# Performance work log

Hardware: AMD Instinct MI355X
Metric: run time of the kernel (lower is better)

Reference implementation:

```python
import jax, jax.numpy as jnp
import numpy as np

B, M, K, KNN = 2, 256, 64, 16
CXYZ, CFEAT = 3, 61
CIN = CXYZ + CFEAT  # 64
MLPS = [64, 128]
SUMM = sum(MLPS)    # 192
CALIB = 64
EXP = [256, 512]
OUT = 256
EPS = 1e-5


def bn(x, g, b):
    # BatchNorm eval mode with running_mean=0, running_var=1 (channel axis 1)
    shape = (1, -1) + (1,) * (x.ndim - 2)
    return x * (g / jnp.sqrt(1.0 + EPS)).reshape(shape) + b.reshape(shape)


def knn(x, k):
    xx = jnp.sum(x * x, axis=1)                      # (B, N)
    inner = jnp.einsum('bcn,bcm->bnm', x, x)         # (B, N, N)
    pd = 2.0 * inner - xx[:, :, None] - xx[:, None, :]
    return jax.lax.top_k(pd, k)[1]                   # (B, N, k)


def graph_feature(x, idx):
    # x: (B, C, N), idx: (B, N, k) -> (B, 2C, N, k)
    xt = jnp.transpose(x, (0, 2, 1))                 # (B, N, C)
    nb = jax.vmap(lambda a, i: a[i])(xt, idx)        # (B, N, k, C)
    ctr = xt[:, :, None, :]
    feat = jnp.concatenate([nb - ctr, jnp.broadcast_to(ctr, nb.shape)], axis=-1)
    return jnp.transpose(feat, (0, 3, 1, 2))


def forward(xyz, feats, e1_w, e1_g, e1_b, e2_w, e2_g, e2_b,
            cal1_w, cal1_g, cal1_b, cal2_w, cal2_bias,
            exp1_w, exp1_g, exp1_b, exp2_w, exp2_g, exp2_b,
            red_w, red_g, red_b, sc1_w, sc1_b, sc2_w, sc2_b,
            sc_n1_g, sc_n1_b, sc_n2_g, sc_n2_b):
    x3 = xyz.reshape(B * M, K, CXYZ).transpose(0, 2, 1)      # (BM, 3, K)
    f = feats.reshape(B * M, K, CFEAT).transpose(0, 2, 1)    # (BM, 61, K)
    idx = knn(x3, KNN)                                        # USE_FEATS_DIS=False: knn once on xyz
    x = jnp.concatenate([x3, f], axis=1)                      # (BM, 64, K)
    outs = []
    for W, g, b in ((e1_w, e1_g, e1_b), (e2_w, e2_g, e2_b)):
        gf = graph_feature(x, idx)                            # (BM, 2C, K, knn)
        y = jax.nn.relu(bn(jnp.einsum('oc,bcnk->bonk', W, gf), g, b))
        x = y.max(axis=-1)                                    # (BM, mlp_i, K)
        outs.append(x)
    x = jnp.concatenate(outs, axis=1)                         # (BM, 192, K)
    c = jax.nn.relu(bn(jnp.einsum('oc,bcn->bon', cal1_w, x), cal1_g, cal1_b))
    c = jnp.einsum('oc,bcn->bon', cal2_w, c) + cal2_bias[None, :, None]
    x = jax.nn.sigmoid(c) * x
    x = jax.nn.relu(bn(jnp.einsum('oc,bcn->bon', exp1_w, x), exp1_g, exp1_b))
    x = jax.nn.relu(bn(jnp.einsum('oc,bcn->bon', exp2_w, x), exp2_g, exp2_b))
    x = x.max(axis=-1).reshape(B, M, EXP[1]).transpose(0, 2, 1)  # (B, 512, M)
    x = jax.nn.relu(bn(jnp.einsum('oc,bcm->bom', red_w, x), red_g, red_b))
    x = bn(x + x, sc_n1_g, sc_n1_b)
    h = jax.nn.relu(jnp.einsum('oc,bcm->bom', sc1_w, x) + sc1_b[None, :, None])
    h = jnp.einsum('oc,bcm->bom', sc2_w, h) + sc2_b[None, :, None]
    x = bn(x + h, sc_n2_g, sc_n2_b)
    return x                                                  # (B, 256, M)


def setup_inputs() -> dict:
    key = jax.random.key(0)
    ks = jax.random.split(key, 16)
    w = lambda k, s: jax.random.normal(k, s, jnp.float32) * 0.05
    ones = lambda n: jnp.ones((n,), jnp.float32)
    zeros = lambda n: jnp.zeros((n,), jnp.float32)
    return {
        'xyz': jax.random.normal(ks[0], (B, M, K, CXYZ), jnp.float32),
        'feats': jax.random.normal(ks[1], (B, M, K, CFEAT), jnp.float32),
        'e1_w': w(ks[2], (MLPS[0], 2 * CIN)), 'e1_g': ones(MLPS[0]), 'e1_b': zeros(MLPS[0]),
        'e2_w': w(ks[3], (MLPS[1], 2 * MLPS[0])), 'e2_g': ones(MLPS[1]), 'e2_b': zeros(MLPS[1]),
        'cal1_w': w(ks[4], (CALIB, SUMM)), 'cal1_g': ones(CALIB), 'cal1_b': zeros(CALIB),
        'cal2_w': w(ks[5], (SUMM, CALIB)), 'cal2_bias': zeros(SUMM),
        'exp1_w': w(ks[6], (EXP[0], SUMM)), 'exp1_g': ones(EXP[0]), 'exp1_b': zeros(EXP[0]),
        'exp2_w': w(ks[7], (EXP[1], EXP[0])), 'exp2_g': ones(EXP[1]), 'exp2_b': zeros(EXP[1]),
        'red_w': w(ks[8], (OUT, EXP[1])), 'red_g': ones(OUT), 'red_b': zeros(OUT),
        'sc1_w': w(ks[9], (OUT, OUT)), 'sc1_b': zeros(OUT),
        'sc2_w': w(ks[10], (OUT, OUT)), 'sc2_b': zeros(OUT),
        'sc_n1_g': ones(OUT), 'sc_n1_b': zeros(OUT),
        'sc_n2_g': ones(OUT), 'sc_n2_b': zeros(OUT),
    }


def reference(xyz, feats, e1_w, e1_g, e1_b, e2_w, e2_g, e2_b,
              cal1_w, cal1_g, cal1_b, cal2_w, cal2_bias,
              exp1_w, exp1_g, exp1_b, exp2_w, exp2_g, exp2_b,
              red_w, red_g, red_b, sc1_w, sc1_b, sc2_w, sc2_b,
              sc_n1_g, sc_n1_b, sc_n2_g, sc_n2_b):
    return forward(xyz, feats, e1_w, e1_g, e1_b, e2_w, e2_g, e2_b,
                   cal1_w, cal1_g, cal1_b, cal2_w, cal2_bias,
                   exp1_w, exp1_g, exp1_b, exp2_w, exp2_g, exp2_b,
                   red_w, red_g, red_b, sc1_w, sc1_b, sc2_w, sc2_b,
                   sc_n1_g, sc_n1_b, sc_n2_g, sc_n2_b)
```

## Files before the change

### kernel.cpp

```cpp
#include <hip/hip_runtime.h>
#include <hip/hip_bf16.h>
#include <math.h>
#include <stddef.h>

#define DEV __device__ __forceinline__
__device__ const float BNS = 0.99999500003749968f;

typedef __bf16 bf16x8 __attribute__((ext_vector_type(8)));
typedef float  f32x4  __attribute__((ext_vector_type(4)));

#define MF(a,b,c) __builtin_amdgcn_mfma_f32_16x16x32_bf16(a,b,c,0,0,0)

DEV unsigned short f2bs(float v){
  union{ __hip_bfloat16 b; unsigned short u; } c; c.b=__float2bfloat16(v); return c.u;
}
DEV float bs2f(unsigned short u){
  union{ unsigned short u; __hip_bfloat16 b; } c; c.u=u; return __bfloat162float(c.b);
}

DEV void put_split4(unsigned short* chunks, int n, int c0, const float* v){
  int cc=c0>>5, u=(c0>>3)&3, e=c0&7;
  unsigned short* base = chunks + cc*4096;
  unsigned short h0=f2bs(v[0]), h1=f2bs(v[1]), h2=f2bs(v[2]), h3=f2bs(v[3]);
  ushort4 hq = make_ushort4(h0,h1,h2,h3);
  ushort4 lq = make_ushort4(f2bs(v[0]-bs2f(h0)), f2bs(v[1]-bs2f(h1)),
                            f2bs(v[2]-bs2f(h2)), f2bs(v[3]-bs2f(h3)));
  *(ushort4*)&base[(n*8 + (u     ^ (n&7)))*8 + e] = hq;
  *(ushort4*)&base[(n*8 + ((u+4) ^ (n&7)))*8 + e] = lq;
}
DEV void get_split4(const unsigned short* chunks, int n, int c0, float* v){
  int cc=c0>>5, u=(c0>>3)&3, e=c0&7;
  const unsigned short* base = chunks + cc*4096;
  ushort4 hq = *(const ushort4*)&base[(n*8 + (u     ^ (n&7)))*8 + e];
  ushort4 lq = *(const ushort4*)&base[(n*8 + ((u+4) ^ (n&7)))*8 + e];
  v[0]=bs2f(hq.x)+bs2f(lq.x); v[1]=bs2f(hq.y)+bs2f(lq.y);
  v[2]=bs2f(hq.z)+bs2f(lq.z); v[3]=bs2f(hq.w)+bs2f(lq.w);
}


__global__ __launch_bounds__(256) void k_prep(const float* __restrict__ e1_w,
    const float* __restrict__ e2_w, const float* __restrict__ cal1_w,
    const float* __restrict__ cal2_w, const float* __restrict__ exp1_w,
    const float* __restrict__ exp2_w, unsigned short* __restrict__ Whi,
    unsigned short* __restrict__ Wlo,
    const float* __restrict__ red_w, const float* __restrict__ sc1_w,
    const float* __restrict__ sc2_w, float* __restrict__ Wt_red,
    float* __restrict__ Wt_s1, float* __restrict__ Wt_s2){
  __shared__ float s[32][33];
  int bid = blockIdx.x;
  if(bid < 896){
    const float* src; unsigned short *hi,*lo; int mode, O=0, i0;
    if(bid<32)      { src=e1_w;  hi=Whi;       lo=Wlo;       mode=1; O= 64; i0=bid*256; }
    else if(bid<96) { src=e2_w;  hi=Whi+8192;  lo=Wlo+8192;  mode=1; O=128; i0=(bid-32)*256; }
    else if(bid<144){ src=cal1_w;hi=Whi+24576; lo=Wlo+24576; mode=0;        i0=(bid-96)*256; }
    else if(bid<192){ src=cal2_w;hi=Whi+36864; lo=Wlo+36864; mode=0;        i0=(bid-144)*256; }
    else if(bid<384){ src=exp1_w;hi=Whi+49152; lo=Wlo+49152; mode=0;        i0=(bid-192)*256; }
    else            { src=exp2_w;hi=Whi+98304; lo=Wlo+98304; mode=0;        i0=(bid-384)*256; }
    int i = i0 + threadIdx.x;
    float v;
    if(mode==0) v = src[i];
    else {
      int row=i>>6, c=i&63;
      v = (row<O) ? src[row*128+c] : (src[(row-O)*128+64+c]-src[(row-O)*128+c]);
    }
    unsigned short h=f2bs(v); hi[i]=h; lo[i]=f2bs(v-bs2f(h));
  } else {
    int lb = bid-896;
    const float* in; float* out; int O,K;
    if(lb<128){ in=red_w; out=Wt_red; O=256; K=512; }
    else if(lb<192){ in=sc1_w; out=Wt_s1; O=256; K=256; lb-=128; }
    else { in=sc2_w; out=Wt_s2; O=256; K=256; lb-=192; }
    int nt=O>>5;
    int to=lb%nt, tk=lb/nt;
    int c=threadIdx.x&31, r8=threadIdx.x>>5;
    #pragma unroll
    for(int p=0;p<4;p++){
      int r=r8+p*8;
      s[r][c]=in[(size_t)(to*32+r)*K + tk*32 + c];
    }
    __syncthreads();
    #pragma unroll
    for(int p=0;p<4;p++){
      int r=r8+p*8;
      out[(size_t)(tk*32+r)*O + to*32 + c]=s[c][r];
    }
  }
}

__global__ __launch_bounds__(256) void k_knne12(const float* __restrict__ xyz,
    const float* __restrict__ feats,
    const unsigned short* __restrict__ W1h, const unsigned short* __restrict__ W1l,
    const unsigned short* __restrict__ W2h, const unsigned short* __restrict__ W2l,
    const float* __restrict__ g1, const float* __restrict__ b1,
    const float* __restrict__ g2, const float* __restrict__ b2,
    unsigned short* __restrict__ cat){
  __shared__ float bufA[64*65];
  __shared__ float bufB[64*65];
  __shared__ __align__(16) unsigned short sb[64*136];
  __shared__ int   ips[64*16];
  __shared__ float sx0[64], sx1[64], sx2[64], sxx[64];
  int bm = blockIdx.x;
  int tid = threadIdx.x, n = tid&63, s = tid>>6;
  int wid = tid>>6, lane = tid&63;
  int l15 = lane&15, q = lane>>4;
  if(s==0){
    const float* xp = xyz + (size_t)(bm*64+n)*3;
    float px=xp[0], py=xp[1], pz=xp[2];
    sx0[n]=px; sx1[n]=py; sx2[n]=pz; sxx[n]=px*px+py*py+pz*pz;
  }
  __syncthreads();
  {
    int p = lane>>2, seg = lane&3;
    int n1 = wid*16 + p;
    float px=sx0[n1], py=sx1[n1], pz=sx2[n1], xxn=sxx[n1];
    float pdr[16];
    #pragma unroll
    for(int t=0;t<16;t++){
      int m = seg*16+t;
      pdr[t] = 2.f*(px*sx0[m]+py*sx1[m]+pz*sx2[m]) - xxn - sxx[m];
    }
    for(int j=0;j<16;j++){
      float bv=-3.4e38f; int bi=seg*16;
      #pragma unroll
      for(int t=0;t<16;t++){ if(pdr[t]>bv){bv=pdr[t]; bi=seg*16+t;} }
      float ov=__shfl_xor(bv,1); int oi=__shfl_xor(bi,1);
      if(ov>bv || (ov==bv && oi<bi)){bv=ov;bi=oi;}
      ov=__shfl_xor(bv,2); oi=__shfl_xor(bi,2);
      if(ov>bv || (ov==bv && oi<bi)){bv=ov;bi=oi;}
      if(seg==0) ips[n1*16+j]=bi;
      if((bi>>4)==seg) pdr[bi&15]=-3.4e38f;
    }
  }
  {
    unsigned short* r = sb + n*136;
    if(s==0){
      float px=sx0[n], py=sx1[n], pz=sx2[n];
      unsigned short h;
      h=f2bs(px); r[0]=h; r[64]=f2bs(px-bs2f(h));
      h=f2bs(py); r[1]=h; r[65]=f2bs(py-bs2f(h));
      h=f2bs(pz); r[2]=h; r[66]=f2bs(pz-bs2f(h));
    }
    const float* fp = feats + (size_t)(bm*64+n)*61;
    #pragma unroll
    for(int t=0;t<16;t++){
      int cc = s*16+t;
      if(cc<61){
        float v=fp[cc]; unsigned short h=f2bs(v);
        r[3+cc]=h; r[64+3+cc]=f2bs(v-bs2f(h));
      }
    }
  }
  __syncthreads();
  {
    int rbase = ((wid<2)?0:64) + (wid&1)*32;
    f32x4 acc[2][4];
    #pragma unroll
    for(int a=0;a<2;a++)
      #pragma unroll
      for(int d=0;d<4;d++) acc[a][d]=(f32x4){0.f,0.f,0.f,0.f};
    #pragma unroll
    for(int kc=0;kc<2;kc++){
      int k0=kc*32;
      size_t a0=(size_t)(rbase+l15)*64 + k0 + q*8;
      size_t a1=(size_t)(rbase+16+l15)*64 + k0 + q*8;
      bf16x8 a0h=*(const bf16x8*)(W1h+a0), a0l=*(const bf16x8*)(W1l+a0);
      bf16x8 a1h=*(const bf16x8*)(W1h+a1), a1l=*(const bf16x8*)(W1l+a1);
      #pragma unroll
      for(int nt=0;nt<4;nt++){
        int row = nt*16 + l15;
        bf16x8 bh = *(const bf16x8*)&sb[row*136 + k0 + q*8];
        bf16x8 bl = *(const bf16x8*)&sb[row*136 + 64 + k0 + q*8];
        acc[0][nt]=MF(a0h,bh,acc[0][nt]);
        acc[0][nt]=MF(a0h,bl,acc[0][nt]);
        acc[0][nt]=MF(a0l,bh,acc[0][nt]);
        acc[1][nt]=MF(a1h,bh,acc[1][nt]);
        acc[1][nt]=MF(a1h,bl,acc[1][nt]);
        acc[1][nt]=MF(a1l,bh,acc[1][nt]);
      }
    }
    __syncthreads();
    float* dst = (wid<2)? bufA : bufB;
    int ro = (wid&1)*32;
    #pragma unroll
    for(int mt=0;mt<2;mt++)
      #pragma unroll
      for(int nt=0;nt<4;nt++)
        #pragma unroll
        for(int rr=0;rr<4;rr++)
          dst[(ro+mt*16+q*4+rr)*65 + nt*16+l15] = acc[mt][nt][rr];
  }
  __syncthreads();
  {
    int o = lane;
    float sc = g1[o]*BNS, bi = b1[o];
    #pragma unroll 4
    for(int j=0;j<16;j++){
      int nn = wid*16 + j;
      const int* ip = &ips[nn*16];
      float mz = -3.4e38f;
      #pragma unroll
      for(int k=0;k<16;k++) mz = fmaxf(mz, bufA[o*65 + ip[k]]);
      float v = fmaxf(sc*(mz + bufB[o*65 + nn]) + bi, 0.f);
      unsigned short hv = f2bs(v), lv = f2bs(v - bs2f(hv));
      size_t cb = ((size_t)bm*64+nn)*384 + o;
      cat[cb] = hv; cat[cb+192] = lv;
      sb[nn*136 + o] = hv; sb[nn*136 + 64 + o] = lv;
    }
  }
  for(int ch=0; ch<2; ch++){
    __syncthreads();
    int rbase = ((wid<2)?0:128) + ch*64 + (wid&1)*32;
    f32x4 acc[2][4];
    #pragma unroll
    for(int a=0;a<2;a++)
      #pragma unroll
      for(int d=0;d<4;d++) acc[a][d]=(f32x4){0.f,0.f,0.f,0.f};
    #pragma unroll
    for(int kc=0;kc<2;kc++){
      int k0=kc*32;
      size_t a0=(size_t)(rbase+l15)*64 + k0 + q*8;
      size_t a1=(size_t)(rbase+16+l15)*64 + k0 + q*8;
      bf16x8 a0h=*(const bf16x8*)(W2h+a0), a0l=*(const bf16x8*)(W2l+a0);
      bf16x8 a1h=*(const bf16x8*)(W2h+a1), a1l=*(const bf16x8*)(W2l+a1);
      #pragma unroll
      for(int nt=0;nt<4;nt++){
        int row = nt*16 + l15;
        bf16x8 bh = *(const bf16x8*)&sb[row*136 + k0 + q*8];
        bf16x8 bl = *(const bf16x8*)&sb[row*136 + 64 + k0 + q*8];
        acc[0][nt]=MF(a0h,bh,acc[0][nt]);
        acc[0][nt]=MF(a0h,bl,acc[0][nt]);
        acc[0][nt]=MF(a0l,bh,acc[0][nt]);
        acc[1][nt]=MF(a1h,bh,acc[1][nt]);
        acc[1][nt]=MF(a1h,bl,acc[1][nt]);
        acc[1][nt]=MF(a1l,bh,acc[1][nt]);
      }
    }
    __syncthreads();
    float* dst = (wid<2)? bufA : bufB;
    int ro = (wid&1)*32;
    #pragma unroll
    for(int mt=0;mt<2;mt++)
      #pragma unroll
      for(int nt=0;nt<4;nt++)
        #pragma unroll
        for(int rr=0;rr<4;rr++)
          dst[(ro+mt*16+q*4+rr)*65 + nt*16+l15] = acc[mt][nt][rr];
    __syncthreads();
    int o = ch*64 + lane;
    float sc = g2[o]*BNS, bi = b2[o];
    #pragma unroll 4
    for(int j=0;j<16;j++){
      int nn = wid*16 + j;
      const int* ip = &ips[nn*16];
      float mz = -3.4e38f;
      #pragma unroll
      for(int k=0;k<16;k++) mz = fmaxf(mz, bufA[lane*65 + ip[k]]);
      float v = fmaxf(sc*(mz + bufB[lane*65 + nn]) + bi, 0.f);
      unsigned short hv = f2bs(v);
      size_t cb = ((size_t)bm*64+nn)*384 + 64 + o;
      cat[cb] = hv; cat[cb+192] = f2bs(v - bs2f(hv));
    }
  }
}

__global__ __launch_bounds__(512,4) void k_mlp(
    const unsigned short* __restrict__ Whi, const unsigned short* __restrict__ Wlo,
    const unsigned short* __restrict__ cats,
    const float* __restrict__ c1g, const float* __restrict__ c1b,
    const float* __restrict__ c2bias,
    const float* __restrict__ e1g, const float* __restrict__ e1b,
    const float* __restrict__ e2g, const float* __restrict__ e2b,
    float* __restrict__ pool){
  __shared__ __align__(16) unsigned short buf[8*4096];
  __shared__ __align__(16) unsigned short calB[2*4096];
  int bm = blockIdx.x;
  int tid = threadIdx.x, wid = tid>>6, lane = tid&63;
  int l15 = lane&15, q = lane>>4;

  const unsigned short* w1h = Whi + 24576;
  const unsigned short* w1l = Wlo + 24576;
  int c1ot = wid>>1, c1rh = wid&1;
  size_t c1wo0 = (size_t)(c1ot*16+l15)*192 + q*8;
  bf16x8 cah = *(const bf16x8*)(w1h+c1wo0);
  bf16x8 cal_ = *(const bf16x8*)(w1l+c1wo0);

  size_t xb = (size_t)bm*24576;
  #pragma unroll
  for(int i=0;i<6;i++){
    int U = tid + i*512;
    int kc = U>>9, w = U&511, rr = w>>3, up = w&7, u = up ^ (rr&7);
    const unsigned short* src = cats + xb + (size_t)rr*384
      + (u<4 ? (kc*32 + u*8) : (192 + kc*32 + (u-4)*8));
    *(uint4*)&buf[kc*4096 + w*8] = *(const uint4*)src;
  }
  __syncthreads();

  f32x4 a0={0.f,0.f,0.f,0.f}, a1={0.f,0.f,0.f,0.f};
  {
    int r0 = c1rh*32+l15, r1 = c1rh*32+16+l15;
    __builtin_amdgcn_s_setprio(1);
    #pragma unroll
    for(int kc=0;kc<6;kc++){
      bf16x8 nah, nal;
      if(kc<5){
        size_t wo = c1wo0 + (kc+1)*32;
        nah=*(const bf16x8*)(w1h+wo); nal=*(const bf16x8*)(w1l+wo);
      }
      const unsigned short* cb = buf + kc*4096;
      bf16x8 xh0=*(const bf16x8*)&cb[(r0*8+((  q)^(r0&7)))*8];
      bf16x8 xl0=*(const bf16x8*)&cb[(r0*8+((4+q)^(r0&7)))*8];
      bf16x8 xh1=*(const bf16x8*)&cb[(r1*8+((  q)^(r1&7)))*8];
      bf16x8 xl1=*(const bf16x8*)&cb[(r1*8+((4+q)^(r1&7)))*8];
      a0=MF(cah,xh0,a0); a1=MF(cah,xh1,a1);
      a0=MF(cah,xl0,a0); a1=MF(cah,xl1,a1);
      a0=MF(cal_,xh0,a0); a1=MF(cal_,xh1,a1);
      cah=nah; cal_=nal;
    }
    __builtin_amdgcn_s_setprio(0);
  }
  const unsigned short* w2h = Whi + 36864;
  const unsigned short* w2l = Wlo + 36864;
  bf16x8 c2h[6], c2l[6];
  #pragma unroll
  for(int i=0;i<6;i++){
    int ot = (wid*6+i)>>2;
    size_t wo=(size_t)(ot*16+l15)*64 + q*8;
    c2h[i]=*(const bf16x8*)(w2h+wo); c2l[i]=*(const bf16x8*)(w2l+wo);
  }
  {
    int c0 = c1ot*16+q*4;
    float4 sg = *(const float4*)&c1g[c0];
    float4 bb = *(const float4*)&c1b[c0];
    float v0[4], v1[4];
    v0[0]=fmaxf(a0[0]*sg.x*BNS+bb.x,0.f); v1[0]=fmaxf(a1[0]*sg.x*BNS+bb.x,0.f);
    v0[1]=fmaxf(a0[1]*sg.y*BNS+bb.y,0.f); v1[1]=fmaxf(a1[1]*sg.y*BNS+bb.y,0.f);
    v0[2]=fmaxf(a0[2]*sg.z*BNS+bb.z,0.f); v1[2]=fmaxf(a1[2]*sg.z*BNS+bb.z,0.f);
    v0[3]=fmaxf(a0[3]*sg.w*BNS+bb.w,0.f); v1[3]=fmaxf(a1[3]*sg.w*BNS+bb.w,0.f);
    put_split4(calB, c1rh*32+l15,    c0, v0);
    put_split4(calB, c1rh*32+16+l15, c0, v1);
  }
  __syncthreads();
  f32x4 ac[6];
  #pragma unroll
  for(int i=0;i<6;i++) ac[i]=(f32x4){0.f,0.f,0.f,0.f};
  #pragma unroll
  for(int kc=0;kc<2;kc++){
    const unsigned short* cb = calB + kc*4096;
    if(kc==1){
      #pragma unroll
      for(int i=0;i<6;i++){
        int ot = (wid*6+i)>>2;
        size_t wo=(size_t)(ot*16+l15)*64 + 32 + q*8;
        c2h[i]=*(const bf16x8*)(w2h+wo); c2l[i]=*(const bf16x8*)(w2l+wo);
      }
    }
    __builtin_amdgcn_s_setprio(1);
    #pragma unroll
    for(int i=0;i<6;i++){
      int nf=(wid*6+i)&3;
      int r=nf*16+l15;
      bf16x8 xh=*(const bf16x8*)&cb[(r*8+((  q)^(r&7)))*8];
      bf16x8 xl=*(const bf16x8*)&cb[(r*8+((4+q)^(r&7)))*8];
      ac[i]=MF(c2h[i],xh,ac[i]); ac[i]=MF(c2h[i],xl,ac[i]); ac[i]=MF(c2l[i],xh,ac[i]);
    }
    __builtin_amdgcn_s_setprio(0);
  }
  const unsigned short* e1wh=Whi+49152; const unsigned short* e1wl=Wlo+49152;
  int ob1 = wid*32;
  bf16x8 p1h[2], p1l[2];
  #pragma unroll
  for(int mt=0;mt<2;mt++){
    size_t wo=(size_t)(ob1+mt*16+l15)*192 + q*8;
    p1h[mt]=*(const bf16x8*)(e1wh+wo); p1l[mt]=*(const bf16x8*)(e1wl+wo);
  }
  #pragma unroll
  for(int i=0;i<6;i++){
    int j=wid*6+i, ot=j>>2, nf=j&3, n=nf*16+l15;
    int c0=ot*16+q*4;
    float4 cb4 = *(const float4*)&c2bias[c0];
    float xv[4];
    get_split4(buf, n, c0, xv);
    xv[0] *= 1.f/(1.f+__expf(-(ac[i][0]+cb4.x)));
    xv[1] *= 1.f/(1.f+__expf(-(ac[i][1]+cb4.y)));
    xv[2] *= 1.f/(1.f+__expf(-(ac[i][2]+cb4.z)));
    xv[3] *= 1.f/(1.f+__expf(-(ac[i][3]+cb4.w)));
    put_split4(buf, n, c0, xv);
  }
  __syncthreads();
  {
    f32x4 e1a[2][4];
    #pragma unroll
    for(int a=0;a<2;a++)
      #pragma unroll
      for(int d=0;d<4;d++) e1a[a][d]=(f32x4){0.f,0.f,0.f,0.f};
    __builtin_amdgcn_s_setprio(1);
    #pragma unroll
    for(int kc=0;kc<6;kc++){
      bf16x8 nh[2], nl[2];
      if(kc<5){
        #pragma unroll
        for(int mt=0;mt<2;mt++){
          size_t wo=(size_t)(ob1+mt*16+l15)*192 + (kc+1)*32 + q*8;
          nh[mt]=*(const bf16x8*)(e1wh+wo); nl[mt]=*(const bf16x8*)(e1wl+wo);
        }
      }
      const unsigned short* cb = buf + kc*4096;
      #pragma unroll
      for(int nf=0;nf<4;nf++){
        int r=nf*16+l15;
        bf16x8 xh=*(const bf16x8*)&cb[(r*8+((  q)^(r&7)))*8];
        bf16x8 xl=*(const bf16x8*)&cb[(r*8+((4+q)^(r&7)))*8];
        e1a[0][nf]=MF(p1h[0],xh,e1a[0][nf]); e1a[1][nf]=MF(p1h[1],xh,e1a[1][nf]);
        e1a[0][nf]=MF(p1h[0],xl,e1a[0][nf]); e1a[1][nf]=MF(p1h[1],xl,e1a[1][nf]);
        e1a[0][nf]=MF(p1l[0],xh,e1a[0][nf]); e1a[1][nf]=MF(p1l[1],xh,e1a[1][nf]);
      }
      p1h[0]=nh[0]; p1h[1]=nh[1]; p1l[0]=nl[0]; p1l[1]=nl[1];
    }
    __builtin_amdgcn_s_setprio(0);
    __syncthreads();
    const unsigned short* e2wh=Whi+98304; const unsigned short* e2wl=Wlo+98304;
    int ob2 = wid*64;
    bf16x8 p2h[4], p2l[4];
    #pragma unroll
    for(int mt=0;mt<4;mt++){
      size_t wo=(size_t)(ob2+mt*16+l15)*256 + q*8;
      p2h[mt]=*(const bf16x8*)(e2wh+wo); p2l[mt]=*(const bf16x8*)(e2wl+wo);
    }
    #pragma unroll
    for(int mt=0;mt<2;mt++){
      int c0 = ob1+mt*16+q*4;
      float4 sg = *(const float4*)&e1g[c0];
      float4 bb = *(const float4*)&e1b[c0];
      #pragma unroll
      for(int nf=0;nf<4;nf++){
        float v[4];
        v[0]=fmaxf(e1a[mt][nf][0]*sg.x*BNS+bb.x,0.f);
        v[1]=fmaxf(e1a[mt][nf][1]*sg.y*BNS+bb.y,0.f);
        v[2]=fmaxf(e1a[mt][nf][2]*sg.z*BNS+bb.z,0.f);
        v[3]=fmaxf(e1a[mt][nf][3]*sg.w*BNS+bb.w,0.f);
        put_split4(buf, nf*16+l15, c0, v);
      }
    }
    __syncthreads();
    f32x4 a2[4][4];
    #pragma unroll
    for(int a=0;a<4;a++)
      #pragma unroll
      for(int d=0;d<4;d++) a2[a][d]=(f32x4){0.f,0.f,0.f,0.f};
    {
      const unsigned short* cb = buf;
      __builtin_amdgcn_s_setprio(1);
      #pragma unroll
      for(int nf=0;nf<4;nf++){
        int r=nf*16+l15;
        bf16x8 xh=*(const bf16x8*)&cb[(r*8+((  q)^(r&7)))*8];
        bf16x8 xl=*(const bf16x8*)&cb[(r*8+((4+q)^(r&7)))*8];
        #pragma unroll
        for(int mt=0;mt<4;mt++) a2[mt][nf]=MF(p2h[mt],xh,a2[mt][nf]);
        #pragma unroll
        for(int mt=0;mt<4;mt++) a2[mt][nf]=MF(p2h[mt],xl,a2[mt][nf]);
        #pragma unroll
        for(int mt=0;mt<4;mt++) a2[mt][nf]=MF(p2l[mt],xh,a2[mt][nf]);
      }
      __builtin_amdgcn_s_setprio(0);
    }
    for(int kc=1;kc<8;kc++){
      bf16x8 ch[4], cl[4];
      #pragma unroll
      for(int mt=0;mt<4;mt++){
        size_t wo=(size_t)(ob2+mt*16+l15)*256 + kc*32 + q*8;
        ch[mt]=*(const bf16x8*)(e2wh+wo); cl[mt]=*(const bf16x8*)(e2wl+wo);
      }
      const unsigned short* cb = buf + kc*4096;
      __builtin_amdgcn_s_setprio(1);
      #pragma unroll
      for(int nf=0;nf<4;nf++){
        int r=nf*16+l15;
        bf16x8 xh=*(const bf16x8*)&cb[(r*8+((  q)^(r&7)))*8];
        bf16x8 xl=*(const bf16x8*)&cb[(r*8+((4+q)^(r&7)))*8];
        #pragma unroll
        for(int mt=0;mt<4;mt++) a2[mt][nf]=MF(ch[mt],xh,a2[mt][nf]);
        #pragma unroll
        for(int mt=0;mt<4;mt++) a2[mt][nf]=MF(ch[mt],xl,a2[mt][nf]);
        #pragma unroll
        for(int mt=0;mt<4;mt++) a2[mt][nf]=MF(cl[mt],xh,a2[mt][nf]);
      }
      __builtin_amdgcn_s_setprio(0);
    }
    int b = bm>>8, m = bm&255;
    #pragma unroll
    for(int mt=0;mt<4;mt++){
      int c0 = ob2+mt*16+q*4;
      float4 sg = *(const float4*)&e2g[c0];
      float4 bb = *(const float4*)&e2b[c0];
      float s[4]={sg.x*BNS,sg.y*BNS,sg.z*BNS,sg.w*BNS};
      float bbv[4]={bb.x,bb.y,bb.z,bb.w};
      #pragma unroll
      for(int rr=0;rr<4;rr++){
        float v = a2[mt][0][rr]*s[rr]+bbv[rr];
        v = fmaxf(v, a2[mt][1][rr]*s[rr]+bbv[rr]);
        v = fmaxf(v, a2[mt][2][rr]*s[rr]+bbv[rr]);
        v = fmaxf(v, a2[mt][3][rr]*s[rr]+bbv[rr]);
        v = fmaxf(v, 0.f);
        v = fmaxf(v, __shfl_xor(v,1));
        v = fmaxf(v, __shfl_xor(v,2));
        v = fmaxf(v, __shfl_xor(v,4));
        v = fmaxf(v, __shfl_xor(v,8));
        if(l15==0) pool[((size_t)b*512 + c0+rr)*256 + m] = v;
      }
    }
  }
}

__global__ __launch_bounds__(512) void k_headf(const float* __restrict__ Wt_red,
    const float* __restrict__ Wt_s1, const float* __restrict__ Wt_s2,
    const float* __restrict__ pool, float* __restrict__ Og,
    const float* __restrict__ red_g, const float* __restrict__ red_b,
    const float* __restrict__ n1g, const float* __restrict__ n1b,
    const float* __restrict__ s1b, const float* __restrict__ s2b,
    const float* __restrict__ n2g, const float* __restrict__ n2b){
  __shared__ float P[512*3];
  __shared__ float X1[256*3];
  __shared__ float H[256*3];
  __shared__ float PB[256*5];
  int g = blockIdx.x;
  int b = g>>7, mg = g&127;
  int m0 = mg*2;
  int tid = threadIdx.x;
  int o = tid&255, h = tid>>8;
  {
    int c = tid;
    float2 v = *(const float2*)&pool[((size_t)b*512+c)*256 + m0];
    P[c*3+0]=v.x; P[c*3+1]=v.y;
  }
  __syncthreads();
  float a0=0.f, a1=0.f;
  {
    int c0 = h*256;
    #pragma unroll 8
    for(int i=0;i<256;i++){
      int c = c0+i;
      float w = Wt_red[c*256+o];
      a0 += w*P[c*3]; a1 += w*P[c*3+1];
    }
  }
  PB[o*5+h*2]=a0; PB[o*5+h*2+1]=a1;
  __syncthreads();
  a0 = PB[o*5]+PB[o*5+2]; a1 = PB[o*5+1]+PB[o*5+3];
  float x0r,x1r;
  {
    float s=red_g[o]*BNS, bi=red_b[o], s1=n1g[o]*BNS, b1=n1b[o];
    float r0=fmaxf(a0*s+bi,0.f), r1=fmaxf(a1*s+bi,0.f);
    x0r=2.f*r0*s1+b1; x1r=2.f*r1*s1+b1;
    if(h==0){ X1[o*3]=x0r; X1[o*3+1]=x1r; }
  }
  __syncthreads();
  a0=0.f; a1=0.f;
  {
    int c0 = h*128;
    #pragma unroll 8
    for(int i=0;i<128;i++){
      int c = c0+i;
      float w = Wt_s1[c*256+o];
      a0 += w*X1[c*3]; a1 += w*X1[c*3+1];
    }
  }
  PB[o*5+h*2]=a0; PB[o*5+h*2+1]=a1;
  __syncthreads();
  a0 = PB[o*5]+PB[o*5+2]; a1 = PB[o*5+1]+PB[o*5+3];
  {
    float bi=s1b[o];
    if(h==0){ H[o*3]=fmaxf(a0+bi,0.f); H[o*3+1]=fmaxf(a1+bi,0.f); }
  }
  __syncthreads();
  a0=0.f; a1=0.f;
  {
    int c0 = h*128;
    #pragma unroll 8
    for(int i=0;i<128;i++){
      int c = c0+i;
      float w = Wt_s2[c*256+o];
      a0 += w*H[c*3]; a1 += w*H[c*3+1];
    }
  }
  PB[o*5+h*2]=a0; PB[o*5+h*2+1]=a1;
  __syncthreads();
  if(h==0){
    a0 = PB[o*5]+PB[o*5+2]; a1 = PB[o*5+1]+PB[o*5+3];
    float bi=s2b[o], s2=n2g[o]*BNS, b2=n2b[o];
    float v0=(x0r+a0+bi)*s2+b2, v1=(x1r+a1+bi)*s2+b2;
    *(float2*)&Og[((size_t)b*256+o)*256 + m0] = make_float2(v0,v1);
  }
}

extern "C" void kernel_launch(void* const* d_in, const int* in_sizes, int n_in,
                              void* d_out, int out_size, void* d_ws, size_t ws_size,
                              hipStream_t stream){
  const float* xyz     =(const float*)d_in[0];
  const float* feats   =(const float*)d_in[1];
  const float* e1_w    =(const float*)d_in[2];
  const float* e1_g    =(const float*)d_in[3];
  const float* e1_b    =(const float*)d_in[4];
  const float* e2_w    =(const float*)d_in[5];
  const float* e2_g    =(const float*)d_in[6];
  const float* e2_b    =(const float*)d_in[7];
  const float* cal1_w  =(const float*)d_in[8];
  const float* cal1_g  =(const float*)d_in[9];
  const float* cal1_b  =(const float*)d_in[10];
  const float* cal2_w  =(const float*)d_in[11];
  const float* cal2_bias=(const float*)d_in[12];
  const float* exp1_w  =(const float*)d_in[13];
  const float* exp1_g  =(const float*)d_in[14];
  const float* exp1_b  =(const float*)d_in[15];
  const float* exp2_w  =(const float*)d_in[16];
  const float* exp2_g  =(const float*)d_in[17];
  const float* exp2_b  =(const float*)d_in[18];
  const float* red_w   =(const float*)d_in[19];
  const float* red_g   =(const float*)d_in[20];
  const float* red_b   =(const float*)d_in[21];
  const float* sc1_w   =(const float*)d_in[22];
  const float* sc1_b   =(const float*)d_in[23];
  const float* sc2_w   =(const float*)d_in[24];
  const float* sc2_b   =(const float*)d_in[25];
  const float* sc_n1_g =(const float*)d_in[26];
  const float* sc_n1_b =(const float*)d_in[27];
  const float* sc_n2_g =(const float*)d_in[28];
  const float* sc_n2_b =(const float*)d_in[29];

  char* wsb=(char*)d_ws;
  unsigned short* cats=(unsigned short*)(wsb + 10485760);
  float*          pool=(float*)         (wsb + 69206016);
  unsigned short* Whi =(unsigned short*)(wsb + 75497472);
  unsigned short* Wlo =(unsigned short*)(wsb + 76021760);
  float*          Wt_red=(float*)       (wsb + 76546048);
  float*          Wt_s1 =(float*)       (wsb + 77070336);
  float*          Wt_s2 =(float*)       (wsb + 77332480);
  unsigned short* e1e_h=Whi;          unsigned short* e1e_l=Wlo;
  unsigned short* e2e_h=Whi+8192;     unsigned short* e2e_l=Wlo+8192;

  k_prep      <<<1152,256,0,stream>>>(e1_w,e2_w,cal1_w,cal2_w,exp1_w,exp2_w,Whi,Wlo,
                                      red_w,sc1_w,sc2_w,Wt_red,Wt_s1,Wt_s2);
  k_knne12    <<<512,256,0,stream>>>(xyz,feats,e1e_h,e1e_l,e2e_h,e2e_l,
                                     e1_g,e1_b,e2_g,e2_b,cats);
  k_mlp       <<<512,512,0,stream>>>(Whi,Wlo,cats,cal1_g,cal1_b,cal2_bias,
                                     exp1_g,exp1_b,exp2_g,exp2_b,pool);
  k_headf     <<<256,512,0,stream>>>(Wt_red,Wt_s1,Wt_s2,pool,(float*)d_out,
                                     red_g,red_b,sc_n1_g,sc_n1_b,sc1_b,sc2_b,sc_n2_g,sc_n2_b);
}
```

Measured before the change: 264.7 us.

## Run kNN/edge-conv kernel with 512 threads and split MFMA correction pass

Doubles k_knne12's block to 512 threads (8 waves). The kNN top-k now uses 8 segments per point with one extra shuffle step, and each wave computes one 16-row MFMA tile instead of two, with half as many points per wave in the max-pool epilogue. This is meant to add latency hiding and parallelism to a kernel that had only 4 waves per block. Separately, the k_mlp exp2 loop now does the low-weight correction MFMAs in a second pass that reloads the high activations from LDS, which may ease register pressure or dependency chains at the cost of extra LDS reads.

```diff
diff --git a/kernel.cpp b/kernel.cpp
--- a/kernel.cpp
+++ b/kernel.cpp
@@ -87,7 +87,7 @@
   }
 }
 
-__global__ __launch_bounds__(256) void k_knne12(const float* __restrict__ xyz,
+__global__ __launch_bounds__(512) void k_knne12(const float* __restrict__ xyz,
     const float* __restrict__ feats,
     const unsigned short* __restrict__ W1h, const unsigned short* __restrict__ W1l,
     const unsigned short* __restrict__ W2h, const unsigned short* __restrict__ W2l,
@@ -110,25 +110,28 @@
   }
   __syncthreads();
   {
-    int p = lane>>2, seg = lane&3;
-    int n1 = wid*16 + p;
+    int p = lane>>3, seg = lane&7;
+    int n1 = wid*8 + p;
     float px=sx0[n1], py=sx1[n1], pz=sx2[n1], xxn=sxx[n1];
-    float pdr[16];
-    #pragma unroll
-    for(int t=0;t<16;t++){
-      int m = seg*16+t;
+    float pdr[8];
+    #pragma unroll
+    for(int t=0;t<8;t++){
+      int m = seg*8+t;
       pdr[t] = 2.f*(px*sx0[m]+py*sx1[m]+pz*sx2[m]) - xxn - sxx[m];
     }
     for(int j=0;j<16;j++){
-      float bv=-3.4e38f; int bi=seg*16;
-      #pragma unroll
-      for(int t=0;t<16;t++){ if(pdr[t]>bv){bv=pdr[t]; bi=seg*16+t;} }
-      float ov=__shfl_xor(bv,1); int oi=__shfl_xor(bi,1);
+      float bv=-3.4e38f; int bi=seg*8;
+      #pragma unroll
+      for(int t=0;t<8;t++){ if(pdr[t]>bv){bv=pdr[t]; bi=seg*8+t;} }
+      float ov; int oi;
+      ov=__shfl_xor(bv,1); oi=__shfl_xor(bi,1);
       if(ov>bv || (ov==bv && oi<bi)){bv=ov;bi=oi;}
       ov=__shfl_xor(bv,2); oi=__shfl_xor(bi,2);
       if(ov>bv || (ov==bv && oi<bi)){bv=ov;bi=oi;}
+      ov=__shfl_xor(bv,4); oi=__shfl_xor(bi,4);
+      if(ov>bv || (ov==bv && oi<bi)){bv=ov;bi=oi;}
       if(seg==0) ips[n1*16+j]=bi;
-      if((bi>>4)==seg) pdr[bi&15]=-3.4e38f;
+      if((bi>>3)==seg) pdr[bi&7]=-3.4e38f;
     }
   }
   {
@@ -142,8 +145,8 @@
     }
     const float* fp = feats + (size_t)(bm*64+n)*61;
     #pragma unroll
-    for(int t=0;t<16;t++){
-      int cc = s*16+t;
+    for(int t=0;t<8;t++){
+      int cc = s*8+t;
       if(cc<61){
         float v=fp[cc]; unsigned short h=f2bs(v);
         r[3+cc]=h; r[64+3+cc]=f2bs(v-bs2f(h));
@@ -152,50 +155,41 @@
   }
   __syncthreads();
   {
-    int rbase = ((wid<2)?0:64) + (wid&1)*32;
-    f32x4 acc[2][4];
-    #pragma unroll
-    for(int a=0;a<2;a++)
-      #pragma unroll
-      for(int d=0;d<4;d++) acc[a][d]=(f32x4){0.f,0.f,0.f,0.f};
+    int rbase = wid*16;
+    f32x4 acc[4];
+    #pragma unroll
+    for(int d=0;d<4;d++) acc[d]=(f32x4){0.f,0.f,0.f,0.f};
     #pragma unroll
     for(int kc=0;kc<2;kc++){
       int k0=kc*32;
       size_t a0=(size_t)(rbase+l15)*64 + k0 + q*8;
-      size_t a1=(size_t)(rbase+16+l15)*64 + k0 + q*8;
       bf16x8 a0h=*(const bf16x8*)(W1h+a0), a0l=*(const bf16x8*)(W1l+a0);
-      bf16x8 a1h=*(const bf16x8*)(W1h+a1), a1l=*(const bf16x8*)(W1l+a1);
       #pragma unroll
       for(int nt=0;nt<4;nt++){
         int row = nt*16 + l15;
         bf16x8 bh = *(const bf16x8*)&sb[row*136 + k0 + q*8];
         bf16x8 bl = *(const bf16x8*)&sb[row*136 + 64 + k0 + q*8];
-        acc[0][nt]=MF(a0h,bh,acc[0][nt]);
-        acc[0][nt]=MF(a0h,bl,acc[0][nt]);
-        acc[0][nt]=MF(a0l,bh,acc[0][nt]);
-        acc[1][nt]=MF(a1h,bh,acc[1][nt]);
-        acc[1][nt]=MF(a1h,bl,acc[1][nt]);
-        acc[1][nt]=MF(a1l,bh,acc[1][nt]);
+        acc[nt]=MF(a0h,bh,acc[nt]);
+        acc[nt]=MF(a0h,bl,acc[nt]);
+        acc[nt]=MF(a0l,bh,acc[nt]);
       }
     }
     __syncthreads();
-    float* dst = (wid<2)? bufA : bufB;
-    int ro = (wid&1)*32;
-    #pragma unroll
-    for(int mt=0;mt<2;mt++)
-      #pragma unroll
-      for(int nt=0;nt<4;nt++)
-        #pragma unroll
-        for(int rr=0;rr<4;rr++)
-          dst[(ro+mt*16+q*4+rr)*65 + nt*16+l15] = acc[mt][nt][rr];
+    float* dst = (wid<4)? bufA : bufB;
+    int ro = (wid&3)*16;
+    #pragma unroll
+    for(int nt=0;nt<4;nt++)
+      #pragma unroll
+      for(int rr=0;rr<4;rr++)
+        dst[(ro+q*4+rr)*65 + nt*16+l15] = acc[nt][rr];
   }
   __syncthreads();
   {
     int o = lane;
     float sc = g1[o]*BNS, bi = b1[o];
     #pragma unroll 4
-    for(int j=0;j<16;j++){
-      int nn = wid*16 + j;
+    for(int j=0;j<8;j++){
+      int nn = wid*8 + j;
       const int* ip = &ips[nn*16];
       float mz = -3.4e38f;
       #pragma unroll
@@ -209,48 +203,39 @@
   }
   for(int ch=0; ch<2; ch++){
     __syncthreads();
-    int rbase = ((wid<2)?0:128) + ch*64 + (wid&1)*32;
-    f32x4 acc[2][4];
-    #pragma unroll
-    for(int a=0;a<2;a++)
-      #pragma unroll
-      for(int d=0;d<4;d++) acc[a][d]=(f32x4){0.f,0.f,0.f,0.f};
+    int wrow = ((wid<4)?0:128) + ch*64 + (wid&3)*16;
+    f32x4 acc[4];
+    #pragma unroll
+    for(int d=0;d<4;d++) acc[d]=(f32x4){0.f,0.f,0.f,0.f};
     #pragma unroll
     for(int kc=0;kc<2;kc++){
       int k0=kc*32;
-      size_t a0=(size_t)(rbase+l15)*64 + k0 + q*8;
-      size_t a1=(size_t)(rbase+16+l15)*64 + k0 + q*8;
+      size_t a0=(size_t)(wrow+l15)*64 + k0 + q*8;
       bf16x8 a0h=*(const bf16x8*)(W2h+a0), a0l=*(const bf16x8*)(W2l+a0);
-      bf16x8 a1h=*(const bf16x8*)(W2h+a1), a1l=*(const bf16x8*)(W2l+a1);
       #pragma unroll
       for(int nt=0;nt<4;nt++){
         int row = nt*16 + l15;
         bf16x8 bh = *(const bf16x8*)&sb[row*136 + k0 + q*8];
         bf16x8 bl = *(const bf16x8*)&sb[row*136 + 64 + k0 + q*8];
-        acc[0][nt]=MF(a0h,bh,acc[0][nt]);
-        acc[0][nt]=MF(a0h,bl,acc[0][nt]);
-        acc[0][nt]=MF(a0l,bh,acc[0][nt]);
-        acc[1][nt]=MF(a1h,bh,acc[1][nt]);
-        acc[1][nt]=MF(a1h,bl,acc[1][nt]);
-        acc[1][nt]=MF(a1l,bh,acc[1][nt]);
+        acc[nt]=MF(a0h,bh,acc[nt]);
+        acc[nt]=MF(a0h,bl,acc[nt]);
+        acc[nt]=MF(a0l,bh,acc[nt]);
       }
     }
     __syncthreads();
-    float* dst = (wid<2)? bufA : bufB;
-    int ro = (wid&1)*32;
-    #pragma unroll
-    for(int mt=0;mt<2;mt++)
-      #pragma unroll
-      for(int nt=0;nt<4;nt++)
-        #pragma unroll
-        for(int rr=0;rr<4;rr++)
-          dst[(ro+mt*16+q*4+rr)*65 + nt*16+l15] = acc[mt][nt][rr];
+    float* dst = (wid<4)? bufA : bufB;
+    int ro = (wid&3)*16;
+    #pragma unroll
+    for(int nt=0;nt<4;nt++)
+      #pragma unroll
+      for(int rr=0;rr<4;rr++)
+        dst[(ro+q*4+rr)*65 + nt*16+l15] = acc[nt][rr];
     __syncthreads();
     int o = ch*64 + lane;
     float sc = g2[o]*BNS, bi = b2[o];
     #pragma unroll 4
-    for(int j=0;j<16;j++){
-      int nn = wid*16 + j;
+    for(int j=0;j<8;j++){
+      int nn = wid*8 + j;
       const int* ip = &ips[nn*16];
       float mz = -3.4e38f;
       #pragma unroll
@@ -482,6 +467,11 @@
         for(int mt=0;mt<4;mt++) a2[mt][nf]=MF(ch[mt],xh,a2[mt][nf]);
         #pragma unroll
         for(int mt=0;mt<4;mt++) a2[mt][nf]=MF(ch[mt],xl,a2[mt][nf]);
+      }
+      #pragma unroll
+      for(int nf=0;nf<4;nf++){
+        int r=nf*16+l15;
+        bf16x8 xh=*(const bf16x8*)&cb[(r*8+((  q)^(r&7)))*8];
         #pragma unroll
         for(int mt=0;mt<4;mt++) a2[mt][nf]=MF(cl[mt],xh,a2[mt][nf]);
       }
@@ -640,7 +630,7 @@
 
   k_prep      <<<1152,256,0,stream>>>(e1_w,e2_w,cal1_w,cal2_w,exp1_w,exp2_w,Whi,Wlo,
                                       red_w,sc1_w,sc2_w,Wt_red,Wt_s1,Wt_s2);
-  k_knne12    <<<512,256,0,stream>>>(xyz,feats,e1e_h,e1e_l,e2e_h,e2e_l,
+  k_knne12    <<<512,512,0,stream>>>(xyz,feats,e1e_h,e1e_l,e2e_h,e2e_l,
                                      e1_g,e1_b,e2_g,e2_b,cats);
   k_mlp       <<<512,512,0,stream>>>(Whi,Wlo,cats,cal1_g,cal1_b,cal2_bias,
                                      exp1_g,exp1_b,exp2_g,exp2_b,pool);
```

Result: no change. 262.4 us (-0.9%).
